# Kernel tuning notes

Hardware: AMD Instinct MI355X
Metric: run time of the kernel (lower is better)

Reference implementation:

```python
import jax, jax.numpy as jnp
import numpy as np

R, N, E, IN_DIM, HID, SEM_H = 3, 50000, 500000, 256, 128, 128


def setup_inputs() -> dict:
    key = jax.random.key(0)
    ks = jax.random.split(key, 20)
    s = 0.05
    return {
        # forward tensor args
        "dst_feat": jax.random.normal(ks[0], (N, IN_DIM), jnp.float32),
        "src_feats": jax.random.normal(ks[1], (R, N, IN_DIM), jnp.float32),
        "src_idx": jax.random.randint(ks[2], (R, E), 0, N, jnp.int32),
        "dst_idx": jax.random.randint(ks[3], (R, E), 0, N, jnp.int32),
        # weight_T: per-ntype projection in_dim -> hidden (dst ntype + R src ntypes, stacked)
        "WT_dst": jax.random.normal(ks[4], (IN_DIM, HID), jnp.float32) * s,
        "bT_dst": jnp.zeros((HID,), jnp.float32),
        "WT_src": jax.random.normal(ks[5], (R, IN_DIM, HID), jnp.float32) * s,
        "bT_src": jnp.zeros((R, HID), jnp.float32),
        # GATConv params per relation (1 head, shared fc for src/dst since in_feats is int)
        "W_gat": jax.random.normal(ks[6], (R, HID, HID), jnp.float32) * s,
        "attn_l": jax.random.normal(ks[7], (R, HID), jnp.float32) * s,
        "attn_r": jax.random.normal(ks[8], (R, HID), jnp.float32) * s,
        "b_gat": jnp.zeros((R, HID), jnp.float32),
        # SemanticAttention: Linear(HID,128)+tanh+Linear(128,1,no bias)
        "W1_sem": jax.random.normal(ks[9], (HID, SEM_H), jnp.float32) * s,
        "b1_sem": jnp.zeros((SEM_H,), jnp.float32),
        "w2_sem": jax.random.normal(ks[10], (SEM_H, 1), jnp.float32) * s,
    }


def reference(dst_feat, src_feats, src_idx, dst_idx,
              WT_dst, bT_dst, WT_src, bT_src,
              W_gat, attn_l, attn_r, b_gat,
              W1_sem, b1_sem, w2_sem):
    # weight_T projections (raw feat dim != hidden_dim branch)
    h_dst = dst_feat @ WT_dst + bT_dst                                  # [N, H]
    h_src = jnp.einsum('rni,rio->rno', src_feats, WT_src) + bT_src[:, None, :]  # [R, N, H]
    n_nodes = h_dst.shape[0]

    def gat(h_s_in, si, di, W, al, ar, b):
        # DGL GATConv, 1 head, eval mode (no dropout), shared fc for src/dst
        hs = h_s_in @ W                                                 # [N, H]
        hd = h_dst @ W                                                  # [N, H]
        el = (hs * al).sum(-1)                                          # [N]
        er = (hd * ar).sum(-1)                                          # [N]
        e = el[si] + er[di]                                             # [E]
        e = jnp.where(e > 0, e, 0.2 * e)                                # leaky_relu(0.2)
        # edge softmax segmented by destination node
        m = jax.ops.segment_max(e, di, num_segments=n_nodes)
        ex = jnp.exp(e - m[di])
        ssum = jax.ops.segment_sum(ex, di, num_segments=n_nodes)
        alpha = ex / ssum[di]                                           # [E]
        out = jax.ops.segment_sum(alpha[:, None] * hs[si], di, num_segments=n_nodes)  # [N, H]
        return jax.nn.elu(out + b)                                      # activation=F.elu, + bias

    z_r = jax.vmap(gat)(h_src, src_idx, dst_idx, W_gat, attn_l, attn_r, b_gat)  # [R, N, H]

    # SemanticAttention over relations
    z_m = jnp.transpose(z_r, (1, 0, 2))                                 # [N, R, H]
    w = jnp.tanh(z_m @ W1_sem + b1_sem) @ w2_sem                        # [N, R, 1]
    a = jax.nn.softmax(w.mean(axis=0), axis=0)                          # [R, 1]
    return (z_m * a).sum(axis=1)                                        # [N, H]
```

## Files before the change

### kernel.cpp

```cpp
#include <hip/hip_runtime.h>
#include <hip/hip_bf16.h>

#define R_REL 3
#define NODE_CHUNK 512
#define BCAP 6144

typedef __attribute__((ext_vector_type(8))) short bf16x8;
typedef __attribute__((ext_vector_type(4))) float f32x4;

static inline size_t align_up(size_t x, size_t a) { return (x + a - 1) & ~(a - 1); }

__device__ __forceinline__ float eluf(float x) {
    return x > 0.f ? x : (__expf(x) - 1.f);
}
__device__ __forceinline__ unsigned short f2bf(float f) {
    __hip_bfloat16 h = __float2bfloat16(f);
    return *reinterpret_cast<unsigned short*>(&h);
}
__device__ __forceinline__ unsigned pk2bf(float lo, float hi) {
    __hip_bfloat162 h = __float22bfloat162_rn(make_float2(lo, hi));
    return *reinterpret_cast<unsigned*>(&h);
}
__device__ __forceinline__ float bf2f(unsigned short h) {
    return __uint_as_float((unsigned)h << 16);
}


__global__ void vu_kernel(const float* __restrict__ W_gat, const float* __restrict__ attn_r,
                          const float* __restrict__ WT_dst, const float* __restrict__ bT_dst,
                          float* __restrict__ u, float* __restrict__ cc) {
    int r = blockIdx.x;
    int t = threadIdx.x;
    __shared__ float ar[128];
    __shared__ float vs[128];
    if (t < 128) ar[t] = attn_r[r * 128 + t];
    __syncthreads();
    if (t < 128) {
        const float* W = W_gat + (size_t)r * 128 * 128 + (size_t)t * 128;
        float s = 0.f;
        for (int j = 0; j < 128; ++j) s += W[j] * ar[j];
        vs[t] = s;
    }
    __syncthreads();
    const float* W = WT_dst + (size_t)t * 128;
    float s = 0.f;
    for (int i = 0; i < 128; ++i) s += W[i] * vs[i];
    u[r * 256 + t] = s;
    if (t == 0) {
        float c = 0.f;
        for (int i = 0; i < 128; ++i) c += bT_dst[i] * vs[i];
        cc[r] = c;
    }
}

__global__ void wc_kernel(const float* __restrict__ WT_src, const float* __restrict__ bT_src,
                          const float* __restrict__ W_gat, float* __restrict__ Wc,
                          float* __restrict__ bc) {
    int r = blockIdx.y;
    int k = blockIdx.x;
    int j = threadIdx.x;
    __shared__ float as[128];
    const float* arow = (k < 256) ? (WT_src + ((size_t)r * 256 + k) * 128)
                                  : (bT_src + (size_t)r * 128);
    as[j] = arow[j];
    __syncthreads();
    const float* W = W_gat + (size_t)r * 128 * 128;
    float s = 0.f;
    for (int i = 0; i < 128; ++i) s += as[i] * W[(size_t)i * 128 + j];
    if (k < 256) Wc[((size_t)r * 256 + k) * 128 + j] = s;
    else         bc[(size_t)r * 128 + j] = s;
}

__global__ void pack_kernel(const float* __restrict__ S, unsigned short* __restrict__ P,
                            int relstride, int KS) {
    int r = blockIdx.y;
    int ks = blockIdx.x >> 3, cb = blockIdx.x & 7;
    int l = threadIdx.x;
    const float* Sr = S + (size_t)r * relstride;
    int col = cb * 16 + (l & 15);
    int kb = ks * 32 + (l >> 4) * 8;
    unsigned short v[8];
#pragma unroll
    for (int j = 0; j < 8; ++j) v[j] = f2bf(Sr[(size_t)(kb + j) * 128 + col]);
    unsigned short* dst = P + ((((size_t)r * KS + ks) * 8 + cb) * 64 + l) * 8;
    *(uint4*)dst = *(uint4*)v;
}


__global__ __launch_bounds__(1024) void gemm_hs(
    const float* __restrict__ src, const unsigned short* __restrict__ Bpack,
    const float* __restrict__ bc, const float* __restrict__ attn_l,
    unsigned short* __restrict__ hsb, float* __restrict__ el, int N) {
    const int r = blockIdx.y;
    const int t = threadIdx.x;
    const int w = t >> 6, l = t & 63;
    __shared__ unsigned short Blds[256 * 128];

    const unsigned short* bsrc = Bpack + (size_t)r * 256 * 128;
#pragma unroll
    for (int i = 0; i < 4; ++i) {
        int c = i * 1024 + t;
        *(uint4*)&Blds[(size_t)c * 8] = *(const uint4*)&bsrc[(size_t)c * 8];
    }
    __syncthreads();

    const int rowbase = blockIdx.x * 256 + w * 16;
    const int arow_i = rowbase + (l & 15);
    const int kg = l >> 4;
    const float* A = src + (size_t)r * N * 256;
    const float* arow = A + (size_t)(arow_i < N ? arow_i : N - 1) * 256;

    f32x4 acc[8] = {};
#pragma unroll
    for (int ks = 0; ks < 8; ++ks) {
        float4 a0 = *(const float4*)(arow + ks * 32 + kg * 8);
        float4 a1 = *(const float4*)(arow + ks * 32 + kg * 8 + 4);
        uint4 uv;
        uv.x = pk2bf(a0.x, a0.y);
        uv.y = pk2bf(a0.z, a0.w);
        uv.z = pk2bf(a1.x, a1.y);
        uv.w = pk2bf(a1.z, a1.w);
        bf16x8 av = *(bf16x8*)&uv;
#pragma unroll
        for (int cf = 0; cf < 8; ++cf) {
            bf16x8 bv = *(const bf16x8*)&Blds[((size_t)(ks * 8 + cf) * 64 + l) * 8];
            acc[cf] = __builtin_amdgcn_mfma_f32_16x16x32_bf16(av, bv, acc[cf], 0, 0, 0);
        }
    }
    float bcv[8], alv[8];
#pragma unroll
    for (int cf = 0; cf < 8; ++cf) {
        int col = cf * 16 + (l & 15);
        bcv[cf] = bc[r * 128 + col];
        alv[cf] = attn_l[r * 128 + col];
    }
#pragma unroll
    for (int i = 0; i < 4; ++i) {
        int row = rowbase + (l >> 4) * 4 + i;
        float pe = 0.f;
        unsigned short hv[8];
#pragma unroll
        for (int cf = 0; cf < 8; ++cf) {
            float v = acc[cf][i] + bcv[cf];
            pe += v * alv[cf];
            hv[cf] = f2bf(v);
        }
        if (row < N) {
            unsigned short* hp = hsb + ((size_t)r * N + row) * 128 + (l & 15);
#pragma unroll
            for (int cf = 0; cf < 8; ++cf) hp[cf * 16] = hv[cf];
        }
        pe += __shfl_xor(pe, 1, 64);
        pe += __shfl_xor(pe, 2, 64);
        pe += __shfl_xor(pe, 4, 64);
        pe += __shfl_xor(pe, 8, 64);
        if ((l & 15) == 0 && row < N) el[(size_t)r * N + row] = pe;
    }
}


__global__ void er_kernel(const float* __restrict__ dst_feat, const float* __restrict__ u,
                          const float* __restrict__ cc, float* __restrict__ er, int N) {
    __shared__ float us[3][256];
    for (int i = threadIdx.x; i < 3 * 256; i += 256) us[i / 256][i & 255] = u[i];
    __syncthreads();
    int wave = threadIdx.x >> 6, lane = threadIdx.x & 63;
    int n = blockIdx.x * 4 + wave;
    if (n >= N) return;
    float4 f = *(const float4*)(dst_feat + (size_t)n * 256 + lane * 4);
#pragma unroll
    for (int r = 0; r < R_REL; ++r) {
        float4 uv = *(float4*)&us[r][lane * 4];
        float s = f.x * uv.x + f.y * uv.y + f.z * uv.z + f.w * uv.w;
#pragma unroll
        for (int off = 32; off >= 1; off >>= 1) s += __shfl_xor(s, off, 64);
        if (lane == 0) er[(size_t)r * N + n] = s + cc[r];
    }
}


__global__ __launch_bounds__(256) void bucket_kernel(
    const int* __restrict__ si, const int* __restrict__ di,
    int* __restrict__ gcnt, unsigned* __restrict__ bbuf, int NB, int E) {
    const int r = blockIdx.y;
    const int t = threadIdx.x;
    const int e0 = blockIdx.x * 1024;
    __shared__ int cnt[128];
    __shared__ int base[128];
    if (t < 128) cnt[t] = 0;
    __syncthreads();
    int bk[4], rank[4]; unsigned pack[4]; bool val[4];
#pragma unroll
    for (int j = 0; j < 4; ++j) {
        int e = e0 + j * 256 + t;
        val[j] = e < E;
        bk[j] = 0; rank[j] = 0; pack[j] = 0;
        if (val[j]) {
            size_t g = (size_t)r * E + e;
            int s = si[g], d = di[g];
            bk[j] = d >> 9;
            pack[j] = (unsigned)s | ((unsigned)d << 16);
            rank[j] = atomicAdd(&cnt[bk[j]], 1);
        }
    }
    __syncthreads();
    if (t < NB && cnt[t] > 0) base[t] = atomicAdd(&gcnt[r * NB + t], cnt[t]);
    __syncthreads();
#pragma unroll
    for (int j = 0; j < 4; ++j) {
        if (val[j])
            bbuf[((size_t)r * NB + bk[j]) * BCAP + base[bk[j]] + rank[j]] = pack[j];
    }
}

__global__ __launch_bounds__(256) void hist_kernel(
    const unsigned* __restrict__ bbuf, const int* __restrict__ gcnt,
    int* __restrict__ deg, int NB, int N) {
    const int r = blockIdx.y;
    const int b = blockIdx.x;
    const int t = threadIdx.x;
    __shared__ int hist[NODE_CHUNK];
    for (int i = t; i < NODE_CHUNK; i += 256) hist[i] = 0;
    __syncthreads();
    const int cnt = gcnt[r * NB + b];
    const unsigned* bb = bbuf + ((size_t)r * NB + b) * BCAP;
    for (int i = t; i < cnt; i += 256) {
        int dloc = (bb[i] >> 16) & (NODE_CHUNK - 1);
        atomicAdd(&hist[dloc], 1);
    }
    __syncthreads();
    for (int i = t; i < NODE_CHUNK; i += 256) {
        int idx = b * NODE_CHUNK + i;
        if (idx < N) deg[(size_t)r * N + idx] = hist[i];
    }
}

__global__ __launch_bounds__(1024) void scan1_kernel(const int* __restrict__ deg,
                                                     int* __restrict__ offs,
                                                     int* __restrict__ btot, int N, int nchunk) {
    const int r = blockIdx.y;
    const int idx = blockIdx.x * 1024 + threadIdx.x;
    const int lane = threadIdx.x & 63, wave = threadIdx.x >> 6;
    __shared__ int wsum[16];
    int v = (idx < N) ? deg[(size_t)r * N + idx] : 0;
    int x = v;
#pragma unroll
    for (int off = 1; off < 64; off <<= 1) {
        int y = __shfl_up(x, off, 64);
        if (lane >= off) x += y;
    }
    if (lane == 63) wsum[wave] = x;
    __syncthreads();
    if (wave == 0 && lane < 16) {
        int y = wsum[lane];
#pragma unroll
        for (int off = 1; off < 16; off <<= 1) {
            int z = __shfl_up(y, off, 64);
            if (lane >= off) y += z;
        }
        wsum[lane] = y;
    }
    __syncthreads();
    int woff = (wave > 0) ? wsum[wave - 1] : 0;
    if (idx < N) offs[(size_t)r * N + idx] = woff + x - v;
    if (threadIdx.x == 1023) btot[r * nchunk + blockIdx.x] = woff + x;
}

__global__ void cscan_kernel(const int* __restrict__ btot, int* __restrict__ cpre, int nchunk) {
    int r = threadIdx.x;
    if (r >= R_REL) return;
    int acc = 0;
    for (int i = 0; i < nchunk; ++i) {
        cpre[r * nchunk + i] = acc;
        acc += btot[r * nchunk + i];
    }
}

__global__ __launch_bounds__(256) void fill2p_kernel(
    const unsigned* __restrict__ bbuf, const int* __restrict__ gcnt,
    const int* __restrict__ offs, const int* __restrict__ cpre,
    const float* __restrict__ el, const float* __restrict__ er,
    uint2* __restrict__ epair, int NB, int nchunk, int N, int E) {
    const int r = blockIdx.y;
    const int b = blockIdx.x;
    const int t = threadIdx.x;
    __shared__ int curl[NODE_CHUNK];
    __shared__ float erl[NODE_CHUNK];
    const int cp = cpre[r * nchunk + (b >> 1)];
    for (int i = t; i < NODE_CHUNK; i += 256) {
        int idx = b * NODE_CHUNK + i;
        curl[i] = (idx < N) ? offs[(size_t)r * N + idx] + cp : 0;
        erl[i]  = (idx < N) ? er[(size_t)r * N + idx] : 0.f;
    }
    __syncthreads();
    const int cnt = gcnt[r * NB + b];
    const unsigned* bb = bbuf + ((size_t)r * NB + b) * BCAP;
    const float* elr = el + (size_t)r * N;
    uint2* epr = epair + (size_t)r * E;
    for (int i = t; i < cnt; i += 256) {
        unsigned pk = bb[i];
        int src = pk & 0xffffu;
        int dloc = (pk >> 16) & (NODE_CHUNK - 1);
        float e = elr[src] + erl[dloc];
        e = e > 0.f ? e : 0.2f * e;
        float p = __expf(e);
        int pos = atomicAdd(&curl[dloc], 1);
        epr[pos] = make_uint2((unsigned)src, __float_as_uint(p));
    }
}


__global__ __launch_bounds__(256) void gather_kernel(
    const uint2* __restrict__ epair, const int* __restrict__ offs,
    const int* __restrict__ cpre, const int* __restrict__ deg,
    const unsigned short* __restrict__ hsb, const float* __restrict__ b_gat,
    unsigned short* __restrict__ z, int N, int E, int nchunk) {
    const int r = blockIdx.y;
    const int t = threadIdx.x;
    const int gid = t >> 4;
    const int gl = t & 15;
    const int d = blockIdx.x * 16 + gid;
    if (d >= N) return;
    const int beg = offs[(size_t)r * N + d] + cpre[r * nchunk + (d >> 10)];
    const int dg = deg[(size_t)r * N + d];
    float ac[8] = {0.f, 0.f, 0.f, 0.f, 0.f, 0.f, 0.f, 0.f};
    float ssum = 0.f;
    const uint2* epr = epair + (size_t)r * E;
    const unsigned short* hsr = hsb + (size_t)r * N * 128;
    int i = beg;
    const int end = beg + dg;
    for (; i + 3 < end; i += 4) {
        uint2 v0 = epr[i], v1 = epr[i + 1], v2 = epr[i + 2], v3 = epr[i + 3];
        uint4 h0 = *(const uint4*)(hsr + (size_t)v0.x * 128 + gl * 8);
        uint4 h1 = *(const uint4*)(hsr + (size_t)v1.x * 128 + gl * 8);
        uint4 h2 = *(const uint4*)(hsr + (size_t)v2.x * 128 + gl * 8);
        uint4 h3 = *(const uint4*)(hsr + (size_t)v3.x * 128 + gl * 8);
        float p0 = __uint_as_float(v0.y), p1 = __uint_as_float(v1.y);
        float p2 = __uint_as_float(v2.y), p3 = __uint_as_float(v3.y);
        ssum += p0 + p1 + p2 + p3;
        ac[0] += p0 * bf2f((unsigned short)(h0.x & 0xffffu)) + p1 * bf2f((unsigned short)(h1.x & 0xffffu))
               + p2 * bf2f((unsigned short)(h2.x & 0xffffu)) + p3 * bf2f((unsigned short)(h3.x & 0xffffu));
        ac[1] += p0 * bf2f((unsigned short)(h0.x >> 16)) + p1 * bf2f((unsigned short)(h1.x >> 16))
               + p2 * bf2f((unsigned short)(h2.x >> 16)) + p3 * bf2f((unsigned short)(h3.x >> 16));
        ac[2] += p0 * bf2f((unsigned short)(h0.y & 0xffffu)) + p1 * bf2f((unsigned short)(h1.y & 0xffffu))
               + p2 * bf2f((unsigned short)(h2.y & 0xffffu)) + p3 * bf2f((unsigned short)(h3.y & 0xffffu));
        ac[3] += p0 * bf2f((unsigned short)(h0.y >> 16)) + p1 * bf2f((unsigned short)(h1.y >> 16))
               + p2 * bf2f((unsigned short)(h2.y >> 16)) + p3 * bf2f((unsigned short)(h3.y >> 16));
        ac[4] += p0 * bf2f((unsigned short)(h0.z & 0xffffu)) + p1 * bf2f((unsigned short)(h1.z & 0xffffu))
               + p2 * bf2f((unsigned short)(h2.z & 0xffffu)) + p3 * bf2f((unsigned short)(h3.z & 0xffffu));
        ac[5] += p0 * bf2f((unsigned short)(h0.z >> 16)) + p1 * bf2f((unsigned short)(h1.z >> 16))
               + p2 * bf2f((unsigned short)(h2.z >> 16)) + p3 * bf2f((unsigned short)(h3.z >> 16));
        ac[6] += p0 * bf2f((unsigned short)(h0.w & 0xffffu)) + p1 * bf2f((unsigned short)(h1.w & 0xffffu))
               + p2 * bf2f((unsigned short)(h2.w & 0xffffu)) + p3 * bf2f((unsigned short)(h3.w & 0xffffu));
        ac[7] += p0 * bf2f((unsigned short)(h0.w >> 16)) + p1 * bf2f((unsigned short)(h1.w >> 16))
               + p2 * bf2f((unsigned short)(h2.w >> 16)) + p3 * bf2f((unsigned short)(h3.w >> 16));
    }
    for (; i < end; ++i) {
        uint2 v = epr[i];
        float p = __uint_as_float(v.y);
        ssum += p;
        uint4 hw = *(const uint4*)(hsr + (size_t)v.x * 128 + gl * 8);
        ac[0] += p * bf2f((unsigned short)(hw.x & 0xffffu));
        ac[1] += p * bf2f((unsigned short)(hw.x >> 16));
        ac[2] += p * bf2f((unsigned short)(hw.y & 0xffffu));
        ac[3] += p * bf2f((unsigned short)(hw.y >> 16));
        ac[4] += p * bf2f((unsigned short)(hw.z & 0xffffu));
        ac[5] += p * bf2f((unsigned short)(hw.z >> 16));
        ac[6] += p * bf2f((unsigned short)(hw.w & 0xffffu));
        ac[7] += p * bf2f((unsigned short)(hw.w >> 16));
    }
    float inv = (dg > 0) ? 1.f / ssum : 0.f;
    const float* bg = b_gat + r * 128 + gl * 8;
    uint4 ow;
    ow.x = pk2bf(eluf(ac[0] * inv + bg[0]), eluf(ac[1] * inv + bg[1]));
    ow.y = pk2bf(eluf(ac[2] * inv + bg[2]), eluf(ac[3] * inv + bg[3]));
    ow.z = pk2bf(eluf(ac[4] * inv + bg[4]), eluf(ac[5] * inv + bg[5]));
    ow.w = pk2bf(eluf(ac[6] * inv + bg[6]), eluf(ac[7] * inv + bg[7]));
    *(uint4*)(z + ((size_t)r * N + d) * 128 + gl * 8) = ow;
}


__global__ __launch_bounds__(256) void gemm_sem(
    const unsigned short* __restrict__ z, const unsigned short* __restrict__ W1p,
    const float* __restrict__ b1, const float* __restrict__ w2,
    float* __restrict__ wpart, int N) {
    const int r = blockIdx.y;
    const int n0 = blockIdx.x * 64;
    const int t = threadIdx.x;
    const int w = t >> 6, l = t & 63;
    __shared__ unsigned short Alds[64 * 128];
    __shared__ float sred[4];
    const unsigned short* A = z + (size_t)r * N * 128;
#pragma unroll
    for (int i = 0; i < 4; ++i) {
        int cid = t + 256 * i;
        int row = cid >> 4, kc = cid & 15;
        uint4 v = make_uint4(0, 0, 0, 0);
        if (n0 + row < N) v = *(const uint4*)(A + (size_t)(n0 + row) * 128 + kc * 8);
        int off = ((row * 256) + kc * 16) ^ ((row & 7) << 4);
        *(uint4*)((char*)Alds + off) = v;
    }
    __syncthreads();

    const bf16x8* bp = (const bf16x8*)W1p;
    f32x4 acc[8] = {};
    const int arow = w * 16 + (l & 15);
#pragma unroll
    for (int ks = 0; ks < 4; ++ks) {
        int aoff = ((arow * 256) + ks * 64 + (l >> 4) * 16) ^ ((arow & 7) << 4);
        bf16x8 av = *(const bf16x8*)((char*)Alds + aoff);
#pragma unroll
        for (int cf = 0; cf < 8; ++cf) {
            bf16x8 bv = bp[(ks * 8 + cf) * 64 + l];
            acc[cf] = __builtin_amdgcn_mfma_f32_16x16x32_bf16(av, bv, acc[cf], 0, 0, 0);
        }
    }
    float b1v[8], w2v[8];
#pragma unroll
    for (int cf = 0; cf < 8; ++cf) {
        int col = cf * 16 + (l & 15);
        b1v[cf] = b1[col];
        w2v[cf] = w2[col];
    }
    float wloc = 0.f;
#pragma unroll
    for (int i = 0; i < 4; ++i) {
        int row = n0 + w * 16 + (l >> 4) * 4 + i;
        float s = 0.f;
#pragma unroll
        for (int cf = 0; cf < 8; ++cf) s += tanhf(acc[cf][i] + b1v[cf]) * w2v[cf];
        s += __shfl_xor(s, 1, 64);
        s += __shfl_xor(s, 2, 64);
        s += __shfl_xor(s, 4, 64);
        s += __shfl_xor(s, 8, 64);
        if ((l & 15) == 0 && row < N) wloc += s;
    }
    wloc += __shfl_xor(wloc, 16, 64);
    wloc += __shfl_xor(wloc, 32, 64);
    if (l == 0) sred[w] = wloc;
    __syncthreads();
    if (t == 0)
        wpart[(size_t)r * gridDim.x + blockIdx.x] = sred[0] + sred[1] + sred[2] + sred[3];
}


__global__ void reduce_sem(const float* __restrict__ wpart, float* __restrict__ aw,
                           int nblk, int N) {
    const int t = threadIdx.x, l = t & 63, w = t >> 6;
    __shared__ float sred[R_REL][4];
    float s[R_REL] = {0.f, 0.f, 0.f};
    for (int i = t; i < nblk; i += 256) {
#pragma unroll
        for (int r = 0; r < R_REL; ++r) s[r] += wpart[(size_t)r * nblk + i];
    }
#pragma unroll
    for (int r = 0; r < R_REL; ++r) {
#pragma unroll
        for (int off = 32; off >= 1; off >>= 1) s[r] += __shfl_xor(s[r], off, 64);
        if (l == 0) sred[r][w] = s[r];
    }
    __syncthreads();
    if (t == 0) {
        float w0 = (sred[0][0] + sred[0][1] + sred[0][2] + sred[0][3]) / (float)N;
        float w1 = (sred[1][0] + sred[1][1] + sred[1][2] + sred[1][3]) / (float)N;
        float w2 = (sred[2][0] + sred[2][1] + sred[2][2] + sred[2][3]) / (float)N;
        float m = fmaxf(w0, fmaxf(w1, w2));
        float e0 = __expf(w0 - m), e1 = __expf(w1 - m), e2 = __expf(w2 - m);
        float si = e0 + e1 + e2;
        aw[0] = e0 / si; aw[1] = e1 / si; aw[2] = e2 / si;
    }
}

__global__ void combine(const unsigned short* __restrict__ z, const float* __restrict__ aw,
                        float* __restrict__ out, int N) {
    int idx = blockIdx.x * 256 + threadIdx.x;
    if (idx >= N * 32) return;
    int n = idx >> 5, c4 = idx & 31;
    float a0 = aw[0], a1 = aw[1], a2 = aw[2];
    uint2 z0 = *(const uint2*)(z + ((size_t)0 * N + n) * 128 + c4 * 4);
    uint2 z1 = *(const uint2*)(z + ((size_t)1 * N + n) * 128 + c4 * 4);
    uint2 z2 = *(const uint2*)(z + ((size_t)2 * N + n) * 128 + c4 * 4);
    float4 o;
    o.x = a0 * bf2f((unsigned short)(z0.x & 0xffffu)) + a1 * bf2f((unsigned short)(z1.x & 0xffffu)) + a2 * bf2f((unsigned short)(z2.x & 0xffffu));
    o.y = a0 * bf2f((unsigned short)(z0.x >> 16))     + a1 * bf2f((unsigned short)(z1.x >> 16))     + a2 * bf2f((unsigned short)(z2.x >> 16));
    o.z = a0 * bf2f((unsigned short)(z0.y & 0xffffu)) + a1 * bf2f((unsigned short)(z1.y & 0xffffu)) + a2 * bf2f((unsigned short)(z2.y & 0xffffu));
    o.w = a0 * bf2f((unsigned short)(z0.y >> 16))     + a1 * bf2f((unsigned short)(z1.y >> 16))     + a2 * bf2f((unsigned short)(z2.y >> 16));
    *(float4*)(out + (size_t)idx * 4) = o;
}


extern "C" void kernel_launch(void* const* d_in, const int* in_sizes, int n_in,
                              void* d_out, int out_size, void* d_ws, size_t ws_size,
                              hipStream_t stream) {
    const float* dst_feat = (const float*)d_in[0];
    const float* src_feats = (const float*)d_in[1];
    const int*   src_idx  = (const int*)d_in[2];
    const int*   dst_idx  = (const int*)d_in[3];
    const float* WT_dst   = (const float*)d_in[4];
    const float* bT_dst   = (const float*)d_in[5];
    const float* WT_src   = (const float*)d_in[6];
    const float* bT_src   = (const float*)d_in[7];
    const float* W_gat    = (const float*)d_in[8];
    const float* attn_l   = (const float*)d_in[9];
    const float* attn_r   = (const float*)d_in[10];
    const float* b_gat    = (const float*)d_in[11];
    const float* W1_sem   = (const float*)d_in[12];
    const float* b1_sem   = (const float*)d_in[13];
    const float* w2_sem   = (const float*)d_in[14];

    const int N = in_sizes[0] / 256;
    const int E = in_sizes[2] / R_REL;
    float* out = (float*)d_out;

    const int nblk = (N + 63) / 64;
    const int nblk_hs = (N + 255) / 256;
    const int nchunk = (N + 1023) / 1024;
    const int NB = (N + NODE_CHUNK - 1) / NODE_CHUNK;

    char* ws = (char*)d_ws;
    size_t off = 0;
    auto alloc = [&](size_t bytes) { char* p = ws + off; off = align_up(off + bytes, 256); return p; };
    unsigned short* hsb   = (unsigned short*)alloc((size_t)R_REL * N * 128 * 2);
    unsigned short* zbuf  = (unsigned short*)alloc((size_t)R_REL * N * 128 * 2);
    float*    Wc    = (float*)alloc((size_t)R_REL * 256 * 128 * 4);
    unsigned short* Wcp   = (unsigned short*)alloc((size_t)R_REL * 256 * 128 * 2);
    unsigned short* W1p   = (unsigned short*)alloc((size_t)128 * 128 * 2);
    float*    bc    = (float*)alloc(R_REL * 128 * 4);
    float*    u     = (float*)alloc(R_REL * 256 * 4);
    float*    cc    = (float*)alloc(R_REL * 4);
    float*    el    = (float*)alloc((size_t)R_REL * N * 4);
    float*    er    = (float*)alloc((size_t)R_REL * N * 4);
    int*      deg   = (int*)alloc((size_t)R_REL * N * 4);
    int*      offs  = (int*)alloc((size_t)R_REL * N * 4);
    int*      btot  = (int*)alloc((size_t)R_REL * nchunk * 4);
    int*      cpre  = (int*)alloc((size_t)R_REL * nchunk * 4);
    int*      gcnt  = (int*)alloc((size_t)R_REL * NB * 4);
    unsigned* bbuf  = (unsigned*)alloc((size_t)R_REL * NB * BCAP * 4);
    uint2*    epair = (uint2*)alloc((size_t)R_REL * E * 8);
    float*    wpart = (float*)alloc((size_t)R_REL * nblk * 4);
    float*    aw    = (float*)alloc(R_REL * 4);

    hipMemsetAsync(gcnt, 0, (size_t)R_REL * NB * 4, stream);

    vu_kernel<<<R_REL, 256, 0, stream>>>(W_gat, attn_r, WT_dst, bT_dst, u, cc);
    wc_kernel<<<dim3(257, R_REL), 128, 0, stream>>>(WT_src, bT_src, W_gat, Wc, bc);
    pack_kernel<<<dim3(64, R_REL), 64, 0, stream>>>(Wc, Wcp, 256 * 128, 8);
    pack_kernel<<<dim3(32, 1), 64, 0, stream>>>(W1_sem, W1p, 0, 4);

    gemm_hs<<<dim3(nblk_hs, R_REL), 1024, 0, stream>>>(src_feats, Wcp, bc, attn_l, hsb, el, N);
    er_kernel<<<(N + 3) / 4, 256, 0, stream>>>(dst_feat, u, cc, er, N);

    bucket_kernel<<<dim3((E + 1023) / 1024, R_REL), 256, 0, stream>>>(src_idx, dst_idx, gcnt, bbuf, NB, E);
    hist_kernel<<<dim3(NB, R_REL), 256, 0, stream>>>(bbuf, gcnt, deg, NB, N);
    scan1_kernel<<<dim3(nchunk, R_REL), 1024, 0, stream>>>(deg, offs, btot, N, nchunk);
    cscan_kernel<<<1, 64, 0, stream>>>(btot, cpre, nchunk);
    fill2p_kernel<<<dim3(NB, R_REL), 256, 0, stream>>>(bbuf, gcnt, offs, cpre, el, er, epair, NB, nchunk, N, E);

    gather_kernel<<<dim3((N + 15) / 16, R_REL), 256, 0, stream>>>(epair, offs, cpre, deg, hsb, b_gat, zbuf, N, E, nchunk);

    gemm_sem<<<dim3(nblk, R_REL), 256, 0, stream>>>(zbuf, W1p, b1_sem, w2_sem, wpart, N);
    reduce_sem<<<1, 256, 0, stream>>>(wpart, aw, nblk, N);
    combine<<<(N * 32 + 255) / 256, 256, 0, stream>>>(zbuf, aw, out, N);
}
```

Before: 245.7 us.

## Fuse histogram, scan and CSR fill into one per-bucket kernel

Replaces the four-kernel CSR build (hist, chunk scan, cross-chunk scan, fill) with a tiny serial scan over bucket counts plus one fused kernel per bucket. That kernel builds the local degree histogram, takes an in-block prefix sum, writes offsets and degrees, and scatters edges. This removes two launches and the global round trips through deg/offs between stages. It also drops the cpre lookup from the gather kernel. The trade-off is a serial single-thread scan over about 98 buckets per relation.

```diff
diff --git a/kernel.cpp b/kernel.cpp
--- a/kernel.cpp
+++ b/kernel.cpp
@@ -213,37 +213,53 @@
     }
 }
 
-__global__ __launch_bounds__(256) void hist_kernel(
+__global__ void bscan_kernel(const int* __restrict__ gcnt, int* __restrict__ bbase, int NB) {
+    int r = threadIdx.x;
+    if (r >= R_REL) return;
+    int acc = 0;
+    for (int i = 0; i < NB; ++i) {
+        bbase[r * NB + i] = acc;
+        acc += gcnt[r * NB + i];
+    }
+}
+
+__global__ __launch_bounds__(256) void fill3_kernel(
     const unsigned* __restrict__ bbuf, const int* __restrict__ gcnt,
-    int* __restrict__ deg, int NB, int N) {
+    const int* __restrict__ bbase, const float* __restrict__ el, const float* __restrict__ er,
+    int* __restrict__ offs, int* __restrict__ deg, uint2* __restrict__ epair,
+    int NB, int N, int E) {
     const int r = blockIdx.y;
     const int b = blockIdx.x;
     const int t = threadIdx.x;
+    const int lane = t & 63, wave = t >> 6;
     __shared__ int hist[NODE_CHUNK];
+    __shared__ int curl[NODE_CHUNK];
+    __shared__ float erl[NODE_CHUNK];
+    __shared__ int wsum[4];
+    __shared__ int wpre[4];
+
     for (int i = t; i < NODE_CHUNK; i += 256) hist[i] = 0;
-    __syncthreads();
+    {
+        int idx0 = b * NODE_CHUNK + t;
+        int idx1 = idx0 + 256;
+        erl[t]       = (idx0 < N) ? er[(size_t)r * N + idx0] : 0.f;
+        erl[t + 256] = (idx1 < N) ? er[(size_t)r * N + idx1] : 0.f;
+    }
+    __syncthreads();
+
     const int cnt = gcnt[r * NB + b];
+    const int bb0 = bbase[r * NB + b];
     const unsigned* bb = bbuf + ((size_t)r * NB + b) * BCAP;
+
     for (int i = t; i < cnt; i += 256) {
         int dloc = (bb[i] >> 16) & (NODE_CHUNK - 1);
         atomicAdd(&hist[dloc], 1);
     }
     __syncthreads();
-    for (int i = t; i < NODE_CHUNK; i += 256) {
-        int idx = b * NODE_CHUNK + i;
-        if (idx < N) deg[(size_t)r * N + idx] = hist[i];
-    }
-}
-
-__global__ __launch_bounds__(1024) void scan1_kernel(const int* __restrict__ deg,
-                                                     int* __restrict__ offs,
-                                                     int* __restrict__ btot, int N, int nchunk) {
-    const int r = blockIdx.y;
-    const int idx = blockIdx.x * 1024 + threadIdx.x;
-    const int lane = threadIdx.x & 63, wave = threadIdx.x >> 6;
-    __shared__ int wsum[16];
-    int v = (idx < N) ? deg[(size_t)r * N + idx] : 0;
-    int x = v;
+
+    int a0 = hist[2 * t], a1 = hist[2 * t + 1];
+    int s = a0 + a1;
+    int x = s;
 #pragma unroll
     for (int off = 1; off < 64; off <<= 1) {
         int y = __shfl_up(x, off, 64);
@@ -251,50 +267,23 @@
     }
     if (lane == 63) wsum[wave] = x;
     __syncthreads();
-    if (wave == 0 && lane < 16) {
-        int y = wsum[lane];
-#pragma unroll
-        for (int off = 1; off < 16; off <<= 1) {
-            int z = __shfl_up(y, off, 64);
-            if (lane >= off) y += z;
-        }
-        wsum[lane] = y;
-    }
-    __syncthreads();
-    int woff = (wave > 0) ? wsum[wave - 1] : 0;
-    if (idx < N) offs[(size_t)r * N + idx] = woff + x - v;
-    if (threadIdx.x == 1023) btot[r * nchunk + blockIdx.x] = woff + x;
-}
-
-__global__ void cscan_kernel(const int* __restrict__ btot, int* __restrict__ cpre, int nchunk) {
-    int r = threadIdx.x;
-    if (r >= R_REL) return;
-    int acc = 0;
-    for (int i = 0; i < nchunk; ++i) {
-        cpre[r * nchunk + i] = acc;
-        acc += btot[r * nchunk + i];
-    }
-}
-
-__global__ __launch_bounds__(256) void fill2p_kernel(
-    const unsigned* __restrict__ bbuf, const int* __restrict__ gcnt,
-    const int* __restrict__ offs, const int* __restrict__ cpre,
-    const float* __restrict__ el, const float* __restrict__ er,
-    uint2* __restrict__ epair, int NB, int nchunk, int N, int E) {
-    const int r = blockIdx.y;
-    const int b = blockIdx.x;
-    const int t = threadIdx.x;
-    __shared__ int curl[NODE_CHUNK];
-    __shared__ float erl[NODE_CHUNK];
-    const int cp = cpre[r * nchunk + (b >> 1)];
-    for (int i = t; i < NODE_CHUNK; i += 256) {
-        int idx = b * NODE_CHUNK + i;
-        curl[i] = (idx < N) ? offs[(size_t)r * N + idx] + cp : 0;
-        erl[i]  = (idx < N) ? er[(size_t)r * N + idx] : 0.f;
-    }
-    __syncthreads();
-    const int cnt = gcnt[r * NB + b];
-    const unsigned* bb = bbuf + ((size_t)r * NB + b) * BCAP;
+    if (t == 0) {
+        int acc = 0;
+#pragma unroll
+        for (int w2 = 0; w2 < 4; ++w2) { wpre[w2] = acc; acc += wsum[w2]; }
+    }
+    __syncthreads();
+    int excl = wpre[wave] + x - s;
+    curl[2 * t] = excl;
+    curl[2 * t + 1] = excl + a0;
+    {
+        int idx0 = b * NODE_CHUNK + 2 * t;
+        if (idx0 < N) { offs[(size_t)r * N + idx0] = bb0 + excl; deg[(size_t)r * N + idx0] = a0; }
+        int idx1 = idx0 + 1;
+        if (idx1 < N) { offs[(size_t)r * N + idx1] = bb0 + excl + a0; deg[(size_t)r * N + idx1] = a1; }
+    }
+    __syncthreads();
+
     const float* elr = el + (size_t)r * N;
     uint2* epr = epair + (size_t)r * E;
     for (int i = t; i < cnt; i += 256) {
@@ -304,7 +293,7 @@
         float e = elr[src] + erl[dloc];
         e = e > 0.f ? e : 0.2f * e;
         float p = __expf(e);
-        int pos = atomicAdd(&curl[dloc], 1);
+        int pos = bb0 + atomicAdd(&curl[dloc], 1);
         epr[pos] = make_uint2((unsigned)src, __float_as_uint(p));
     }
 }
@@ -312,16 +301,15 @@
 
 __global__ __launch_bounds__(256) void gather_kernel(
     const uint2* __restrict__ epair, const int* __restrict__ offs,
-    const int* __restrict__ cpre, const int* __restrict__ deg,
-    const unsigned short* __restrict__ hsb, const float* __restrict__ b_gat,
-    unsigned short* __restrict__ z, int N, int E, int nchunk) {
+    const int* __restrict__ deg, const unsigned short* __restrict__ hsb,
+    const float* __restrict__ b_gat, unsigned short* __restrict__ z, int N, int E) {
     const int r = blockIdx.y;
     const int t = threadIdx.x;
     const int gid = t >> 4;
     const int gl = t & 15;
     const int d = blockIdx.x * 16 + gid;
     if (d >= N) return;
-    const int beg = offs[(size_t)r * N + d] + cpre[r * nchunk + (d >> 10)];
+    const int beg = offs[(size_t)r * N + d];
     const int dg = deg[(size_t)r * N + d];
     float ac[8] = {0.f, 0.f, 0.f, 0.f, 0.f, 0.f, 0.f, 0.f};
     float ssum = 0.f;
@@ -514,7 +502,6 @@
 
     const int nblk = (N + 63) / 64;
     const int nblk_hs = (N + 255) / 256;
-    const int nchunk = (N + 1023) / 1024;
     const int NB = (N + NODE_CHUNK - 1) / NODE_CHUNK;
 
     char* ws = (char*)d_ws;
@@ -532,9 +519,8 @@
     float*    er    = (float*)alloc((size_t)R_REL * N * 4);
     int*      deg   = (int*)alloc((size_t)R_REL * N * 4);
     int*      offs  = (int*)alloc((size_t)R_REL * N * 4);
-    int*      btot  = (int*)alloc((size_t)R_REL * nchunk * 4);
-    int*      cpre  = (int*)alloc((size_t)R_REL * nchunk * 4);
     int*      gcnt  = (int*)alloc((size_t)R_REL * NB * 4);
+    int*      bbase = (int*)alloc((size_t)R_REL * NB * 4);
     unsigned* bbuf  = (unsigned*)alloc((size_t)R_REL * NB * BCAP * 4);
     uint2*    epair = (uint2*)alloc((size_t)R_REL * E * 8);
     float*    wpart = (float*)alloc((size_t)R_REL * nblk * 4);
@@ -551,12 +537,10 @@
     er_kernel<<<(N + 3) / 4, 256, 0, stream>>>(dst_feat, u, cc, er, N);
 
     bucket_kernel<<<dim3((E + 1023) / 1024, R_REL), 256, 0, stream>>>(src_idx, dst_idx, gcnt, bbuf, NB, E);
-    hist_kernel<<<dim3(NB, R_REL), 256, 0, stream>>>(bbuf, gcnt, deg, NB, N);
-    scan1_kernel<<<dim3(nchunk, R_REL), 1024, 0, stream>>>(deg, offs, btot, N, nchunk);
-    cscan_kernel<<<1, 64, 0, stream>>>(btot, cpre, nchunk);
-    fill2p_kernel<<<dim3(NB, R_REL), 256, 0, stream>>>(bbuf, gcnt, offs, cpre, el, er, epair, NB, nchunk, N, E);
-
-    gather_kernel<<<dim3((N + 15) / 16, R_REL), 256, 0, stream>>>(epair, offs, cpre, deg, hsb, b_gat, zbuf, N, E, nchunk);
+    bscan_kernel<<<1, 64, 0, stream>>>(gcnt, bbase, NB);
+    fill3_kernel<<<dim3(NB, R_REL), 256, 0, stream>>>(bbuf, gcnt, bbase, el, er, offs, deg, epair, NB, N, E);
+
+    gather_kernel<<<dim3((N + 15) / 16, R_REL), 256, 0, stream>>>(epair, offs, deg, hsb, b_gat, zbuf, N, E);
 
     gemm_sem<<<dim3(nblk, R_REL), 256, 0, stream>>>(zbuf, W1p, b1_sem, w2_sem, wpart, N);
     reduce_sem<<<1, 256, 0, stream>>>(wpart, aw, nblk, N);
```

New measurement: 244.3 us. No clear change (-0.6%).
